# Optimization experiments

Measured on AMD Instinct MI355X. Metric: run time of the kernel, lower is better.

## Reference

```python
import jax, jax.numpy as jnp
import numpy as np

N_DOMAIN, D_IN, UNITS, LORA_R = 64, 256, 128, 4
BATCH = 131072


def setup_inputs() -> dict:
    key = jax.random.key(0)
    ks = jax.random.split(key, 7)
    x = jax.random.normal(ks[0], (BATCH, D_IN), dtype=jnp.float32)
    domain_indicator = jax.random.randint(ks[1], (BATCH, 1), 0, N_DOMAIN, dtype=jnp.int32)
    a_kernel = jax.random.normal(ks[2], (N_DOMAIN, D_IN, LORA_R), dtype=jnp.float32) * 0.05
    b_kernel = jax.random.normal(ks[3], (N_DOMAIN, LORA_R, UNITS), dtype=jnp.float32) * 0.05
    domain_bias = jax.random.normal(ks[4], (N_DOMAIN, UNITS), dtype=jnp.float32) * 0.05
    kernel = jax.random.normal(ks[5], (D_IN, UNITS), dtype=jnp.float32) * 0.05
    bias = jax.random.normal(ks[6], (UNITS,), dtype=jnp.float32) * 0.05
    return {"x": x, "domain_indicator": domain_indicator, "a_kernel": a_kernel,
            "b_kernel": b_kernel, "domain_bias": domain_bias, "kernel": kernel, "bias": bias}


def reference(x, domain_indicator, a_kernel, b_kernel, domain_bias, kernel, bias):
    # shared dense path (dropout is identity at inference)
    out = x @ kernel + bias  # [B, units]
    # domain index: original uses domain_indicator[0, 0] (one domain per batch)
    idx = domain_indicator[0, 0]
    A = a_kernel[idx]        # [d_in, r]
    B = b_kernel[idx]        # [r, units]
    db = domain_bias[idx]    # [units]
    out = out + (x @ A) @ B + db
    return jax.nn.relu(out)
```

## Files before the change

kernel.cpp:

```cpp
#include <hip/hip_runtime.h>
#include <hip/hip_bf16.h>

#define D_IN   256
#define UNITS  128
#define LORA_R 4
#define ROWS_PER_TILE   16
#define TILES_PER_BLOCK 4
#define GRID_GEMM       2048

typedef __attribute__((ext_vector_type(8))) short short8;
typedef __attribute__((ext_vector_type(4))) float f32x4;

static __device__ __forceinline__ unsigned short f2bf(float f) {
    unsigned u = __float_as_uint(f);
    unsigned r = (u + 0x7FFFu + ((u >> 16) & 1u)) >> 16;
    return (unsigned short)r;
}

static __device__ __forceinline__ void gll16(const void* g, void* l) {
    __builtin_amdgcn_global_load_lds(
        (const __attribute__((address_space(1))) unsigned int*)g,
        (__attribute__((address_space(3))) unsigned int*)l,
        16, 0, 0);
}

__global__ void mlora_prep(const float* __restrict__ a_kernel,
                           const float* __restrict__ b_kernel,
                           const float* __restrict__ domain_bias,
                           const float* __restrict__ kernel,
                           const float* __restrict__ bias,
                           const int* __restrict__ dom,
                           unsigned short* __restrict__ wfrag,
                           float* __restrict__ bias_eff) {
    const int idx = dom[0];
    const int tid = blockIdx.x * 256 + threadIdx.x;
    const int n = tid & (UNITS - 1);
    const int k = tid >> 7;
    const float* __restrict__ A = a_kernel + (size_t)idx * D_IN * LORA_R;
    const float* __restrict__ B = b_kernel + (size_t)idx * LORA_R * UNITS;
    float w = kernel[k * UNITS + n];
#pragma unroll
    for (int r = 0; r < LORA_R; ++r) w += A[k * LORA_R + r] * B[r * UNITS + n];
    const int s = k >> 5, g = (k >> 3) & 3, j = k & 7;
    const int t = n >> 4, lo = n & 15;
    const int lane = g * 16 + lo;
    wfrag[(size_t)((s * 8 + t) * 64 + lane) * 8 + j] = f2bf(w);
    if (tid < UNITS) bias_eff[tid] = bias[tid] + domain_bias[idx * UNITS + tid];
}

__global__ __launch_bounds__(256, 4) void mlora_gemm(
    const float* __restrict__ x,
    const unsigned short* __restrict__ wfrag,
    const float* __restrict__ bias_eff,
    float* __restrict__ out) {
    __shared__ float lds[2][ROWS_PER_TILE * 256];
    const int lane = threadIdx.x & 63;
    const int wave = threadIdx.x >> 6;
    const int t0 = wave * 2;
    const int rlo = lane & 15;
    const int g = lane >> 4;

    short8 bfrag[8][2];
#pragma unroll
    for (int s = 0; s < 8; ++s) {
#pragma unroll
        for (int tt = 0; tt < 2; ++tt) {
            bfrag[s][tt] = *reinterpret_cast<const short8*>(
                wfrag + (size_t)((s * 8 + t0 + tt) * 64 + lane) * 8);
        }
    }
    const float b0 = bias_eff[t0 * 16 + rlo];
    const float b1 = bias_eff[(t0 + 1) * 16 + rlo];

    const size_t block_row0 = (size_t)blockIdx.x * (ROWS_PER_TILE * TILES_PER_BLOCK);

#define STAGE(bufi, tile)                                                     \
    do {                                                                      \
        const char* gbase = (const char*)x +                                  \
            (block_row0 + (size_t)(tile) * ROWS_PER_TILE + wave * 4) * 1024;  \
        char* lbase = (char*)&lds[bufi][wave * 4 * 256];                      \
        _Pragma("unroll")                                                     \
        for (int i = 0; i < 4; ++i) {                                         \
            const int rsw = (wave * 4 + i) & 7;                               \
            gll16(gbase + i * 1024 + ((lane * 16) ^ (rsw << 4)),              \
                  lbase + i * 1024);                                          \
        }                                                                     \
    } while (0)

    STAGE(0, 0);
    __syncthreads();

    for (int t = 0; t < TILES_PER_BLOCK; ++t) {
        const int buf = t & 1;
        if (t + 1 < TILES_PER_BLOCK) STAGE(buf ^ 1, t + 1);

        const size_t r0g = block_row0 + (size_t)t * ROWS_PER_TILE;
        const int swz = (rlo & 7) << 4;
        const char* lrow = (const char*)&lds[buf][rlo * 256];
        f32x4 acc0 = {0.f, 0.f, 0.f, 0.f};
        f32x4 acc1 = {0.f, 0.f, 0.f, 0.f};
#pragma unroll
        for (int s = 0; s < 8; ++s) {
            const int base = s * 128 + g * 32;
            f32x4 u0 = *reinterpret_cast<const f32x4*>(lrow + (base ^ swz));
            f32x4 u1 = *reinterpret_cast<const f32x4*>(lrow + ((base + 16) ^ swz));
            union { short8 s8; __hip_bfloat162 h2[4]; } af;
            af.h2[0] = __float22bfloat162_rn(make_float2(u0[0], u0[1]));
            af.h2[1] = __float22bfloat162_rn(make_float2(u0[2], u0[3]));
            af.h2[2] = __float22bfloat162_rn(make_float2(u1[0], u1[1]));
            af.h2[3] = __float22bfloat162_rn(make_float2(u1[2], u1[3]));
            acc0 = __builtin_amdgcn_mfma_f32_16x16x32_bf16(af.s8, bfrag[s][0], acc0, 0, 0, 0);
            acc1 = __builtin_amdgcn_mfma_f32_16x16x32_bf16(af.s8, bfrag[s][1], acc1, 0, 0, 0);
        }
        float* op = out + (r0g + g * 4) * UNITS;
#pragma unroll
        for (int j = 0; j < 4; ++j) {
            op[(size_t)j * UNITS + t0 * 16 + rlo]      = fmaxf(acc0[j] + b0, 0.f);
            op[(size_t)j * UNITS + t0 * 16 + 16 + rlo] = fmaxf(acc1[j] + b1, 0.f);
        }
        __syncthreads();
    }
#undef STAGE
}

extern "C" void kernel_launch(void* const* d_in, const int* in_sizes, int n_in,
                              void* d_out, int out_size, void* d_ws, size_t ws_size,
                              hipStream_t stream) {
    const float* x           = (const float*)d_in[0];
    const int*   dom         = (const int*)d_in[1];
    const float* a_kernel    = (const float*)d_in[2];
    const float* b_kernel    = (const float*)d_in[3];
    const float* domain_bias = (const float*)d_in[4];
    const float* kernel      = (const float*)d_in[5];
    const float* bias        = (const float*)d_in[6];
    float* out = (float*)d_out;

    unsigned short* wfrag = (unsigned short*)d_ws;
    float* bias_eff = (float*)((char*)d_ws + 65536);

    mlora_prep<<<128, 256, 0, stream>>>(a_kernel, b_kernel, domain_bias,
                                        kernel, bias, dom, wfrag, bias_eff);
    mlora_gemm<<<GRID_GEMM, 256, 0, stream>>>(x, wfrag, bias_eff, out);
}
```

Baseline: 41.11 us.

## Drop in-block double buffering; one 16-row tile per block with 4x grid

Replaces the four-tile, double-buffered LDS pipeline in each block with a single 16-row tile per block, and quadruples the grid to 8192 blocks. LDS use per block halves and the launch bound asks for 5 blocks per CU, so overlap is meant to come from running more resident blocks rather than from software pipelining. The cost is that every block reloads the full B-fragment set (64 KB of weights) from global/L2 for only 16 rows, which means more weight traffic and more block launch overhead.

New measurement: 44.92 us. 9.3% more time.

```diff
diff --git a/kernel.cpp b/kernel.cpp
--- a/kernel.cpp
+++ b/kernel.cpp
@@ -4,9 +4,7 @@
 #define D_IN   256
 #define UNITS  128
 #define LORA_R 4
-#define ROWS_PER_TILE   16
-#define TILES_PER_BLOCK 4
-#define GRID_GEMM       2048
+#define GRID_GEMM 8192
 
 typedef __attribute__((ext_vector_type(8))) short short8;
 typedef __attribute__((ext_vector_type(4))) float f32x4;
@@ -48,12 +46,12 @@
     if (tid < UNITS) bias_eff[tid] = bias[tid] + domain_bias[idx * UNITS + tid];
 }
 
-__global__ __launch_bounds__(256, 4) void mlora_gemm(
+__global__ __launch_bounds__(256, 5) void mlora_gemm(
     const float* __restrict__ x,
     const unsigned short* __restrict__ wfrag,
     const float* __restrict__ bias_eff,
     float* __restrict__ out) {
-    __shared__ float lds[2][ROWS_PER_TILE * 256];
+    __shared__ float lds[16 * 256];
     const int lane = threadIdx.x & 63;
     const int wave = threadIdx.x >> 6;
     const int t0 = wave * 2;
@@ -72,55 +70,40 @@
     const float b0 = bias_eff[t0 * 16 + rlo];
     const float b1 = bias_eff[(t0 + 1) * 16 + rlo];
 
-    const size_t block_row0 = (size_t)blockIdx.x * (ROWS_PER_TILE * TILES_PER_BLOCK);
-
-#define STAGE(bufi, tile)                                                     \
-    do {                                                                      \
-        const char* gbase = (const char*)x +                                  \
-            (block_row0 + (size_t)(tile) * ROWS_PER_TILE + wave * 4) * 1024;  \
-        char* lbase = (char*)&lds[bufi][wave * 4 * 256];                      \
-        _Pragma("unroll")                                                     \
-        for (int i = 0; i < 4; ++i) {                                         \
-            const int rsw = (wave * 4 + i) & 7;                               \
-            gll16(gbase + i * 1024 + ((lane * 16) ^ (rsw << 4)),              \
-                  lbase + i * 1024);                                          \
-        }                                                                     \
-    } while (0)
-
-    STAGE(0, 0);
+    const size_t row0 = (size_t)blockIdx.x * 16;
+    const char* gbase = (const char*)x + (row0 + wave * 4) * 1024;
+    char* lbase = (char*)lds + (size_t)wave * 4 * 1024;
+#pragma unroll
+    for (int i = 0; i < 4; ++i) {
+        const int rsw = (wave * 4 + i) & 7;
+        gll16(gbase + (size_t)i * 1024 + ((lane * 16) ^ (rsw << 4)),
+              lbase + (size_t)i * 1024);
+    }
     __syncthreads();
 
-    for (int t = 0; t < TILES_PER_BLOCK; ++t) {
-        const int buf = t & 1;
-        if (t + 1 < TILES_PER_BLOCK) STAGE(buf ^ 1, t + 1);
-
-        const size_t r0g = block_row0 + (size_t)t * ROWS_PER_TILE;
-        const int swz = (rlo & 7) << 4;
-        const char* lrow = (const char*)&lds[buf][rlo * 256];
-        f32x4 acc0 = {0.f, 0.f, 0.f, 0.f};
-        f32x4 acc1 = {0.f, 0.f, 0.f, 0.f};
+    const int swz = (rlo & 7) << 4;
+    const char* lrow = (const char*)lds + (size_t)rlo * 1024;
+    f32x4 acc0 = {0.f, 0.f, 0.f, 0.f};
+    f32x4 acc1 = {0.f, 0.f, 0.f, 0.f};
 #pragma unroll
-        for (int s = 0; s < 8; ++s) {
-            const int base = s * 128 + g * 32;
-            f32x4 u0 = *reinterpret_cast<const f32x4*>(lrow + (base ^ swz));
-            f32x4 u1 = *reinterpret_cast<const f32x4*>(lrow + ((base + 16) ^ swz));
-            union { short8 s8; __hip_bfloat162 h2[4]; } af;
-            af.h2[0] = __float22bfloat162_rn(make_float2(u0[0], u0[1]));
-            af.h2[1] = __float22bfloat162_rn(make_float2(u0[2], u0[3]));
-            af.h2[2] = __float22bfloat162_rn(make_float2(u1[0], u1[1]));
-            af.h2[3] = __float22bfloat162_rn(make_float2(u1[2], u1[3]));
-            acc0 = __builtin_amdgcn_mfma_f32_16x16x32_bf16(af.s8, bfrag[s][0], acc0, 0, 0, 0);
-            acc1 = __builtin_amdgcn_mfma_f32_16x16x32_bf16(af.s8, bfrag[s][1], acc1, 0, 0, 0);
-        }
-        float* op = out + (r0g + g * 4) * UNITS;
+    for (int s = 0; s < 8; ++s) {
+        const int base = s * 128 + g * 32;
+        f32x4 u0 = *reinterpret_cast<const f32x4*>(lrow + (base ^ swz));
+        f32x4 u1 = *reinterpret_cast<const f32x4*>(lrow + ((base + 16) ^ swz));
+        union { short8 s8; __hip_bfloat162 h2[4]; } af;
+        af.h2[0] = __float22bfloat162_rn(make_float2(u0[0], u0[1]));
+        af.h2[1] = __float22bfloat162_rn(make_float2(u0[2], u0[3]));
+        af.h2[2] = __float22bfloat162_rn(make_float2(u1[0], u1[1]));
+        af.h2[3] = __float22bfloat162_rn(make_float2(u1[2], u1[3]));
+        acc0 = __builtin_amdgcn_mfma_f32_16x16x32_bf16(af.s8, bfrag[s][0], acc0, 0, 0, 0);
+        acc1 = __builtin_amdgcn_mfma_f32_16x16x32_bf16(af.s8, bfrag[s][1], acc1, 0, 0, 0);
+    }
+    float* op = out + (row0 + g * 4) * UNITS;
 #pragma unroll
-        for (int j = 0; j < 4; ++j) {
-            op[(size_t)j * UNITS + t0 * 16 + rlo]      = fmaxf(acc0[j] + b0, 0.f);
-            op[(size_t)j * UNITS + t0 * 16 + 16 + rlo] = fmaxf(acc1[j] + b1, 0.f);
-        }
-        __syncthreads();
+    for (int j = 0; j < 4; ++j) {
+        op[(size_t)j * UNITS + t0 * 16 + rlo]      = fmaxf(acc0[j] + b0, 0.f);
+        op[(size_t)j * UNITS + t0 * 16 + 16 + rlo] = fmaxf(acc1[j] + b1, 0.f);
     }
-#undef STAGE
 }
 
 extern "C" void kernel_launch(void* const* d_in, const int* in_sizes, int n_in,
```
